# Kernel tuning notes

Measured on AMD Instinct MI355X. Metric: run time of the kernel, lower is better.

The kernel has to match this reference:

```python
import jax, jax.numpy as jnp
import numpy as np

T = 1000
NUM_CLASSES = 100
BATCH = 256


def setup_inputs() -> dict:
    key = jax.random.key(0)
    k_mu, k_ls, k_eps, k_y = jax.random.split(key, 4)
    mu = jax.random.normal(k_mu, (BATCH, NUM_CLASSES), dtype=jnp.float32)
    log_sigma2 = jax.random.normal(k_ls, (BATCH, NUM_CLASSES), dtype=jnp.float32)
    # MVN(0, I) samples == i.i.d. standard normals; materialized for determinism.
    eps = jax.random.normal(k_eps, (T, BATCH, NUM_CLASSES), dtype=jnp.float32)
    y = jax.random.randint(k_y, (BATCH,), 0, NUM_CLASSES, dtype=jnp.int64)
    return {"mu": mu, "log_sigma2": log_sigma2, "eps": eps, "y": y}


def reference(mu, log_sigma2, eps, y):
    t = eps.shape[0]
    log_T = jnp.asarray(np.log(t), dtype=mu.dtype)
    sigma = jnp.exp(0.5 * log_sigma2)  # [B, C]
    logits = mu[None, :, :] + sigma[None, :, :] * eps  # [T, B, C]
    # per-sample log-probabilities, weighted by 1/T in log-space
    y_hat = jax.nn.log_softmax(logits, axis=-1) - log_T  # [T, B, C]
    log_p = jax.nn.logsumexp(y_hat, axis=0)  # [B, C]
    # nll_loss with mean reduction: -mean over batch of log_p at true class
    picked = jnp.take_along_axis(log_p, y[:, None], axis=1)[:, 0]  # [B]
    return -jnp.mean(picked)
```

## Files before the change

### kernel.cpp

```cpp
#include <hip/hip_runtime.h>

#define T_TOT 1000
#define NCLS  100
#define BATCH 256
#define LOG_T 6.90775527898213705f
#define GRID  2048

__global__ __launch_bounds__(256) void rows_kernel(const float* __restrict__ mu,
                                                   const float* __restrict__ ls2,
                                                   const float* __restrict__ eps,
                                                   const int* __restrict__ y,
                                                   float* __restrict__ v_ws) {
    const int lane = threadIdx.x & 63;
    const int half = lane >> 5;
    const int j    = lane & 31;
    const int wid  = (blockIdx.x * 256 + threadIdx.x) >> 6;
    const int nw   = (GRID * 256) >> 6;
    const int total_pairs = (T_TOT * BATCH) / 2;

    const int b = (2 * wid + half) & (BATCH - 1);
    const int yb = y[b];
    const int ks = yb & 3;
    const int owner = yb >> 2;

    float4 m4 = make_float4(0.f, 0.f, 0.f, 0.f);
    float4 s4 = m4;
    if (j < 25) {
        m4 = *(const float4*)(mu  + b * NCLS + 4 * j);
        const float4 l4 = *(const float4*)(ls2 + b * NCLS + 4 * j);
        s4.x = __expf(0.5f * l4.x);
        s4.y = __expf(0.5f * l4.y);
        s4.z = __expf(0.5f * l4.z);
        s4.w = __expf(0.5f * l4.w);
    }

    for (int pair = wid; pair < total_pairs; pair += nw) {
        const int r = pair * 2 + half;
        const int t = r >> 8;

        float x0 = -INFINITY, x1 = -INFINITY, x2 = -INFINITY, x3 = -INFINITY;
        if (j < 25) {
            const float4 e4 = *(const float4*)(eps + (size_t)r * NCLS + 4 * j);
            x0 = fmaf(s4.x, e4.x, m4.x);
            x1 = fmaf(s4.y, e4.y, m4.y);
            x2 = fmaf(s4.z, e4.z, m4.z);
            x3 = fmaf(s4.w, e4.w, m4.w);
        }

        float s = __expf(x0) + __expf(x1) + __expf(x2) + __expf(x3);
        #pragma unroll
        for (int off = 1; off <= 16; off <<= 1)
            s += __shfl_xor(s, off, 64);

        if (j == owner) {
            const float px = (ks == 0) ? x0 : (ks == 1) ? x1 : (ks == 2) ? x2 : x3;
            v_ws[b * T_TOT + t] = px - __logf(s);
        }
    }
}

__global__ __launch_bounds__(1024) void lse_kernel(const float* __restrict__ v_ws,
                                                   float* __restrict__ out) {
    const int tid = threadIdx.x;
    const int w = tid >> 6;
    const int l = tid & 63;

    float acc = 0.f;
    for (int b = w; b < BATCH; b += 16) {
        const float4* vb = (const float4*)(v_ws + b * T_TOT);
        const float4 ninf = make_float4(-INFINITY, -INFINITY, -INFINITY, -INFINITY);
        const float4 a0 = (l       < 250) ? vb[l]       : ninf;
        const float4 a1 = (l + 64  < 250) ? vb[l + 64]  : ninf;
        const float4 a2 = (l + 128 < 250) ? vb[l + 128] : ninf;
        const float4 a3 = (l + 192 < 250) ? vb[l + 192] : ninf;

        float m = fmaxf(fmaxf(fmaxf(a0.x, a0.y), fmaxf(a0.z, a0.w)),
                        fmaxf(fmaxf(a1.x, a1.y), fmaxf(a1.z, a1.w)));
        m = fmaxf(m, fmaxf(fmaxf(fmaxf(a2.x, a2.y), fmaxf(a2.z, a2.w)),
                           fmaxf(fmaxf(a3.x, a3.y), fmaxf(a3.z, a3.w))));
        #pragma unroll
        for (int off = 1; off <= 32; off <<= 1) m = fmaxf(m, __shfl_xor(m, off, 64));

        float s = __expf(a0.x - m) + __expf(a0.y - m) + __expf(a0.z - m) + __expf(a0.w - m)
                + __expf(a1.x - m) + __expf(a1.y - m) + __expf(a1.z - m) + __expf(a1.w - m)
                + __expf(a2.x - m) + __expf(a2.y - m) + __expf(a2.z - m) + __expf(a2.w - m)
                + __expf(a3.x - m) + __expf(a3.y - m) + __expf(a3.z - m) + __expf(a3.w - m);
        #pragma unroll
        for (int off = 1; off <= 32; off <<= 1) s += __shfl_xor(s, off, 64);

        acc += m + __logf(s);
    }

    __shared__ float red[16];
    if (l == 0) red[w] = acc;
    __syncthreads();
    if (tid == 0) {
        float tot = 0.f;
        #pragma unroll
        for (int i = 0; i < 16; ++i) tot += red[i];
        out[0] = LOG_T - tot * (1.0f / BATCH);
    }
}

extern "C" void kernel_launch(void* const* d_in, const int* in_sizes, int n_in,
                              void* d_out, int out_size, void* d_ws, size_t ws_size,
                              hipStream_t stream) {
    const float* mu  = (const float*)d_in[0];
    const float* ls2 = (const float*)d_in[1];
    const float* eps = (const float*)d_in[2];
    const int*   y   = (const int*)d_in[3];
    float* out  = (float*)d_out;
    float* v_ws = (float*)d_ws;

    rows_kernel<<<GRID, 256, 0, stream>>>(mu, ls2, eps, y, v_ws);
    lse_kernel<<<1, 1024, 0, stream>>>(v_ws, out);
}
```

Baseline: 174.3 us.

## Accumulate per-row softmax probabilities in registers instead of storing log-probs for LSE

Each wave now sums exp(log-softmax) for its fixed batch row across the time steps it visits and writes one partial sum per row-slot. The final kernel just adds 64 partials per row and takes a log, replacing the max-stabilised logsumexp over 1000 stored values. This removes the 1 MB intermediate write/read and makes the tail kernel cheaper. It drops max-subtraction, which is safe here because probabilities are at most 1, but it costs an extra exp per row in the main loop.

```diff
diff --git a/kernel.cpp b/kernel.cpp
--- a/kernel.cpp
+++ b/kernel.cpp
@@ -10,7 +10,7 @@
                                                    const float* __restrict__ ls2,
                                                    const float* __restrict__ eps,
                                                    const int* __restrict__ y,
-                                                   float* __restrict__ v_ws) {
+                                                   float* __restrict__ partial) {
     const int lane = threadIdx.x & 63;
     const int half = lane >> 5;
     const int j    = lane & 31;
@@ -18,7 +18,8 @@
     const int nw   = (GRID * 256) >> 6;
     const int total_pairs = (T_TOT * BATCH) / 2;
 
-    const int b = (2 * wid + half) & (BATCH - 1);
+    const int h = 2 * wid + half;
+    const int b = h & (BATCH - 1);
     const int yb = y[b];
     const int ks = yb & 3;
     const int owner = yb >> 2;
@@ -34,9 +35,9 @@
         s4.w = __expf(0.5f * l4.w);
     }
 
+    float acc = 0.f;
     for (int pair = wid; pair < total_pairs; pair += nw) {
         const int r = pair * 2 + half;
-        const int t = r >> 8;
 
         float x0 = -INFINITY, x1 = -INFINITY, x2 = -INFINITY, x3 = -INFINITY;
         if (j < 25) {
@@ -54,50 +55,33 @@
 
         if (j == owner) {
             const float px = (ks == 0) ? x0 : (ks == 1) ? x1 : (ks == 2) ? x2 : x3;
-            v_ws[b * T_TOT + t] = px - __logf(s);
+            acc += __expf(px - __logf(s));
         }
     }
+
+    if (j == owner) partial[b * 64 + (h >> 8)] = acc;
 }
 
-__global__ __launch_bounds__(1024) void lse_kernel(const float* __restrict__ v_ws,
-                                                   float* __restrict__ out) {
-    const int tid = threadIdx.x;
-    const int w = tid >> 6;
-    const int l = tid & 63;
+__global__ __launch_bounds__(256) void final_kernel(const float* __restrict__ partial,
+                                                    float* __restrict__ out) {
+    const int b = threadIdx.x;
+    const float4* p4 = (const float4*)(partial + b * 64);
+    float s = 0.f;
+    #pragma unroll
+    for (int i = 0; i < 16; ++i) {
+        const float4 a = p4[i];
+        s += (a.x + a.y) + (a.z + a.w);
+    }
+    float lg = __logf(s);
 
-    float acc = 0.f;
-    for (int b = w; b < BATCH; b += 16) {
-        const float4* vb = (const float4*)(v_ws + b * T_TOT);
-        const float4 ninf = make_float4(-INFINITY, -INFINITY, -INFINITY, -INFINITY);
-        const float4 a0 = (l       < 250) ? vb[l]       : ninf;
-        const float4 a1 = (l + 64  < 250) ? vb[l + 64]  : ninf;
-        const float4 a2 = (l + 128 < 250) ? vb[l + 128] : ninf;
-        const float4 a3 = (l + 192 < 250) ? vb[l + 192] : ninf;
+    #pragma unroll
+    for (int off = 1; off <= 32; off <<= 1) lg += __shfl_xor(lg, off, 64);
 
-        float m = fmaxf(fmaxf(fmaxf(a0.x, a0.y), fmaxf(a0.z, a0.w)),
-                        fmaxf(fmaxf(a1.x, a1.y), fmaxf(a1.z, a1.w)));
-        m = fmaxf(m, fmaxf(fmaxf(fmaxf(a2.x, a2.y), fmaxf(a2.z, a2.w)),
-                           fmaxf(fmaxf(a3.x, a3.y), fmaxf(a3.z, a3.w))));
-        #pragma unroll
-        for (int off = 1; off <= 32; off <<= 1) m = fmaxf(m, __shfl_xor(m, off, 64));
-
-        float s = __expf(a0.x - m) + __expf(a0.y - m) + __expf(a0.z - m) + __expf(a0.w - m)
-                + __expf(a1.x - m) + __expf(a1.y - m) + __expf(a1.z - m) + __expf(a1.w - m)
-                + __expf(a2.x - m) + __expf(a2.y - m) + __expf(a2.z - m) + __expf(a2.w - m)
-                + __expf(a3.x - m) + __expf(a3.y - m) + __expf(a3.z - m) + __expf(a3.w - m);
-        #pragma unroll
-        for (int off = 1; off <= 32; off <<= 1) s += __shfl_xor(s, off, 64);
-
-        acc += m + __logf(s);
-    }
-
-    __shared__ float red[16];
-    if (l == 0) red[w] = acc;
+    __shared__ float red[4];
+    if ((b & 63) == 0) red[b >> 6] = lg;
     __syncthreads();
-    if (tid == 0) {
-        float tot = 0.f;
-        #pragma unroll
-        for (int i = 0; i < 16; ++i) tot += red[i];
+    if (b == 0) {
+        const float tot = (red[0] + red[1]) + (red[2] + red[3]);
         out[0] = LOG_T - tot * (1.0f / BATCH);
     }
 }
@@ -109,9 +93,9 @@
     const float* ls2 = (const float*)d_in[1];
     const float* eps = (const float*)d_in[2];
     const int*   y   = (const int*)d_in[3];
-    float* out  = (float*)d_out;
-    float* v_ws = (float*)d_ws;
+    float* out     = (float*)d_out;
+    float* partial = (float*)d_ws;
 
-    rows_kernel<<<GRID, 256, 0, stream>>>(mu, ls2, eps, y, v_ws);
-    lse_kernel<<<1, 1024, 0, stream>>>(v_ws, out);
+    rows_kernel<<<GRID, 256, 0, stream>>>(mu, ls2, eps, y, partial);
+    final_kernel<<<1, 256, 0, stream>>>(partial, out);
 }
```

Result: faster. 155.3 us (-10.9%).
